# Kernel tuning notes

Measured on AMD Instinct MI355X. Metric: run time of the kernel, lower is better.

The kernel has to match this reference:

```python
import jax, jax.numpy as jnp
import numpy as np

D_MODEL = 128
H = 256          # lstm_hidden_dim
L = 2            # lstm_num_layers
PRED_LEN = 45
OUT_DIM = 2
B = 4096


def _glorot(key, shape):
    fan = shape[-1]
    return jax.random.uniform(key, shape, jnp.float32, -1.0, 1.0) / jnp.sqrt(jnp.float32(fan))


def setup_inputs() -> dict:
    key = jax.random.key(0)
    ks = jax.random.split(key, 20)
    inp = {
        "encoder_feat": jax.random.normal(ks[0], (B, D_MODEL), jnp.float32),
        "last_obs_pos": jax.random.normal(ks[1], (B, OUT_DIM), jnp.float32),
        "context": jax.random.normal(ks[2], (B, D_MODEL), jnp.float32),
        # hidden/cell init projections: Linear(d_model -> H*L)
        "Wh_init": _glorot(ks[3], (H * L, D_MODEL)),
        "bh_init": jnp.zeros((H * L,), jnp.float32),
        "Wc_init": _glorot(ks[4], (H * L, D_MODEL)),
        "bc_init": jnp.zeros((H * L,), jnp.float32),
        # LSTM layer 0: input = OUT_DIM + D_MODEL
        "W_ih0": _glorot(ks[5], (4 * H, OUT_DIM + D_MODEL)),
        "W_hh0": _glorot(ks[6], (4 * H, H)),
        "b_ih0": jnp.zeros((4 * H,), jnp.float32),
        "b_hh0": jnp.zeros((4 * H,), jnp.float32),
        # LSTM layer 1: input = H
        "W_ih1": _glorot(ks[7], (4 * H, H)),
        "W_hh1": _glorot(ks[8], (4 * H, H)),
        "b_ih1": jnp.zeros((4 * H,), jnp.float32),
        "b_hh1": jnp.zeros((4 * H,), jnp.float32),
        # output_proj: Linear(H,64) -> ReLU -> Linear(64, OUT_DIM)
        "Wp1": _glorot(ks[9], (64, H)),
        "bp1": jnp.zeros((64,), jnp.float32),
        "Wp2": _glorot(ks[10], (OUT_DIM, 64)),
        "bp2": jnp.zeros((OUT_DIM,), jnp.float32),
    }
    return inp


def _lstm_cell(gates_x, h, c, W_hh):
    # gates_x already = x @ W_ih.T + b_ih + b_hh ; torch gate order: i, f, g, o
    gates = gates_x + h @ W_hh.T
    i, f, g, o = jnp.split(gates, 4, axis=-1)
    c_new = jax.nn.sigmoid(f) * c + jax.nn.sigmoid(i) * jnp.tanh(g)
    h_new = jax.nn.sigmoid(o) * jnp.tanh(c_new)
    return h_new, c_new


def reference(encoder_feat, last_obs_pos, context,
              Wh_init, bh_init, Wc_init, bc_init,
              W_ih0, W_hh0, b_ih0, b_hh0,
              W_ih1, W_hh1, b_ih1, b_hh1,
              Wp1, bp1, Wp2, bp2):
    b = encoder_feat.shape[0]
    # init hidden/cell: [B, L*H] -> per-layer [B, H]
    h_all = (encoder_feat @ Wh_init.T + bh_init).reshape(b, L, H)
    c_all = (encoder_feat @ Wc_init.T + bc_init).reshape(b, L, H)
    h0, h1 = h_all[:, 0], h_all[:, 1]
    c0, c1 = c_all[:, 0], c_all[:, 1]

    # context is constant across steps: precompute its gate contribution once
    bias0 = b_ih0 + b_hh0
    gates_ctx = context @ W_ih0[:, OUT_DIM:].T + bias0   # [B, 4H]
    W_pos = W_ih0[:, :OUT_DIM]                            # [4H, 2]
    bias1 = b_ih1 + b_hh1

    def step(carry, _):
        pos, h0, c0, h1, c1 = carry
        gates_x0 = gates_ctx + pos @ W_pos.T
        h0, c0 = _lstm_cell(gates_x0, h0, c0, W_hh0)
        gates_x1 = h0 @ W_ih1.T + bias1
        h1, c1 = _lstm_cell(gates_x1, h1, c1, W_hh1)
        delta = jax.nn.relu(h1 @ Wp1.T + bp1) @ Wp2.T + bp2
        pos = pos + delta
        return (pos, h0, c0, h1, c1), pos

    _, traj = jax.lax.scan(step, (last_obs_pos, h0, c0, h1, c1), None, length=PRED_LEN)
    return jnp.transpose(traj, (1, 0, 2))  # [B, pred_len, 2]
```

## Files before the change

### kernel.cpp

```cpp
#include <hip/hip_runtime.h>


#define HN    256
#define DM    128
#define NSTEP 45

#define H0A_OFF  1605632ULL
#define HBUF_B   2097152ULL
#define H0B_OFF  (H0A_OFF + HBUF_B)
#define H1A_OFF  (H0B_OFF + HBUF_B)
#define H1B_OFF  (H1A_OFF + HBUF_B)
#define GX_OFF   (H1B_OFF + HBUF_B)
#define GX_B     8388608ULL
#define C0_OFF   (GX_OFF + GX_B)
#define CB_B     4194304ULL
#define C1_OFF   (C0_OFF + CB_B)
#define POSA_OFF (C1_OFF + CB_B)
#define POSB_OFF (POSA_OFF + 32768ULL)
#define WS_NEED  (POSB_OFF + 32768ULL)

typedef __attribute__((ext_vector_type(8))) short s8v;
typedef __attribute__((ext_vector_type(4))) float f32x4;

#define MFMA16(a,b,c) __builtin_amdgcn_mfma_f32_16x16x32_bf16((a),(b),(c),0,0,0)

__device__ __forceinline__ unsigned short f2bf(float f){
  union { float f; unsigned u; } x; x.f = f;
  unsigned r = x.u + 0x7fffu + ((x.u >> 16) & 1u);
  return (unsigned short)(r >> 16);
}
__device__ __forceinline__ float bf2f(unsigned short h){
  union { unsigned u; float f; } x; x.u = ((unsigned)h) << 16;
  return x.f;
}
__device__ __forceinline__ float sigm(float x){
  x = fminf(40.f, fmaxf(-40.f, x));
  return 1.f/(1.f + __expf(-x));
}
__device__ __forceinline__ float tanhx(float x){
  float xx = fminf(15.f, fmaxf(-15.f, x));
  float e = __expf(2.f*xx);
  return (e-1.f)/(e+1.f);
}

__device__ __forceinline__ void store_h(unsigned short* buf, int blk, int b, int u, float v){
  buf[(size_t)blk*4096 + (u>>5)*512 + ((b&15) + ((u>>3)&3)*16)*8 + (u&7)] = f2bf(v);
}
__device__ __forceinline__ s8v ld_af(const unsigned short* buf, int blk, int kt, int lane){
  return *(const s8v*)(buf + (size_t)blk*4096 + kt*512 + lane*8);
}

__global__ void repack(const float* __restrict__ Whh0, const float* __restrict__ Wih1,
                       const float* __restrict__ Whh1, const float* __restrict__ Wp1,
                       unsigned short* __restrict__ dst){
  int gid  = blockIdx.x*256 + threadIdx.x;
  int lane = gid & 63;
  int tile = gid >> 6;
  const float* src; int row; size_t doff;
  int k0 = (lane>>4)*8;
  if (tile < 1536){
    int mi = tile / 512;
    int r  = tile % 512;
    int ut = r & 15;
    int kt = (r >> 4) & 7;
    int g  = r >> 7;
    src  = (mi==0) ? Whh0 : (mi==1) ? Wih1 : Whh1;
    row  = g*256 + ut*16 + (lane&15);
    k0  += kt*32;
    doff = (size_t)mi*262144 + (size_t)r*512 + lane*8;
  } else {
    int r2 = tile - 1536;
    int kt = r2 & 7, pt = r2 >> 3;
    src  = Wp1;
    row  = pt*16 + (lane&15);
    k0  += kt*32;
    doff = 786432 + (size_t)r2*512 + lane*8;
  }
  const float* s = src + (size_t)row*HN + k0;
  float4 a = *(const float4*)(s);
  float4 b = *(const float4*)(s+4);
  unsigned short* d = dst + doff;
  d[0]=f2bf(a.x); d[1]=f2bf(a.y); d[2]=f2bf(a.z); d[3]=f2bf(a.w);
  d[4]=f2bf(b.x); d[5]=f2bf(b.y); d[6]=f2bf(b.z); d[7]=f2bf(b.w);
}

__global__ __launch_bounds__(512, 1)
void k_init(const float* __restrict__ enc, const float* __restrict__ pos0,
            const float* __restrict__ ctx, const float* __restrict__ Wh,
            const float* __restrict__ bh,  const float* __restrict__ Wc,
            const float* __restrict__ bc,  const float* __restrict__ Wih0,
            const float* __restrict__ bih0,const float* __restrict__ bhh0,
            unsigned short* __restrict__ h0a, unsigned short* __restrict__ h1a,
            unsigned short* __restrict__ gxg,
            float* __restrict__ c0g, float* __restrict__ c1g,
            float* __restrict__ posg)
{
  __shared__ float sh_x[16*DM];
  const int tid = threadIdx.x;
  const int blk = blockIdx.x;
  const int gb0 = blk*16;

  {
    const float4* src = (const float4*)(enc + (size_t)gb0*DM);
    ((float4*)sh_x)[tid] = src[tid];
  }
  if (tid < 32) posg[(size_t)gb0*2 + tid] = pos0[(size_t)gb0*2 + tid];
  __syncthreads();

  {
    const int r = tid;
    float ah[16], ac[16];
    #pragma unroll
    for (int b=0;b<16;b++){ ah[b]=0.f; ac[b]=0.f; }
    const float4* whr = (const float4*)(Wh + (size_t)r*DM);
    const float4* wcr = (const float4*)(Wc + (size_t)r*DM);
    #pragma unroll 4
    for (int kk=0; kk<DM/4; kk++){
      float4 w0 = whr[kk], w1 = wcr[kk];
      #pragma unroll
      for (int b=0;b<16;b++){
        float4 x = *(const float4*)&sh_x[b*DM + kk*4];
        ah[b] += w0.x*x.x + w0.y*x.y + w0.z*x.z + w0.w*x.w;
        ac[b] += w1.x*x.x + w1.y*x.y + w1.z*x.z + w1.w*x.w;
      }
    }
    float bhv = bh[r], bcv = bc[r];
    if (r < HN){
      #pragma unroll
      for (int b=0;b<16;b++){
        store_h(h0a, blk, b, r, ah[b] + bhv);
        c0g[(size_t)blk*4096 + r*16 + b] = ac[b] + bcv;
      }
    } else {
      #pragma unroll
      for (int b=0;b<16;b++){
        store_h(h1a, blk, b, r-HN, ah[b] + bhv);
        c1g[(size_t)blk*4096 + (r-HN)*16 + b] = ac[b] + bcv;
      }
    }
  }
  __syncthreads();

  {
    const float4* src = (const float4*)(ctx + (size_t)gb0*DM);
    ((float4*)sh_x)[tid] = src[tid];
  }
  __syncthreads();

  {
    float a0[16], a1[16];
    #pragma unroll
    for (int b=0;b<16;b++){ a0[b]=0.f; a1[b]=0.f; }
    const float2* wr0 = (const float2*)(Wih0 + (size_t)tid*130 + 2);
    const float2* wr1 = (const float2*)(Wih0 + (size_t)(tid+512)*130 + 2);
    #pragma unroll 4
    for (int kk=0; kk<DM/2; kk++){
      float2 w0 = wr0[kk], w1 = wr1[kk];
      #pragma unroll
      for (int b=0;b<16;b++){
        float2 x = *(const float2*)&sh_x[b*DM + kk*2];
        a0[b] += w0.x*x.x + w0.y*x.y;
        a1[b] += w1.x*x.x + w1.y*x.y;
      }
    }
    float cb0 = bih0[tid]     + bhh0[tid];
    float cb1 = bih0[tid+512] + bhh0[tid+512];
    #pragma unroll
    for (int b=0;b<16;b++){
      gxg[(size_t)blk*16384 + (size_t)tid*16 + b]       = f2bf(a0[b] + cb0);
      gxg[(size_t)blk*16384 + (size_t)(tid+512)*16 + b] = f2bf(a1[b] + cb1);
    }
  }
}

__global__ __launch_bounds__(512, 1)
void k_layer0(const unsigned short* __restrict__ wsW,
              const unsigned short* __restrict__ gxg,
              const unsigned short* __restrict__ h0rd,
              unsigned short* __restrict__ h0wr,
              const unsigned short* __restrict__ h1prev,
              float* __restrict__ c0g,
              const float* __restrict__ posRd,
              float* __restrict__ posWr,
              const float* __restrict__ Wih0,
              const float* __restrict__ bp1,
              const float* __restrict__ Wp2,
              const float* __restrict__ bp2,
              float* __restrict__ out, int t)
{
  const int tid  = threadIdx.x;
  const int lane = tid & 63;
  const int w    = tid >> 6;
  const int wb   = w >> 1;
  const int wh   = w & 1;
  const int col  = lane & 15;
  const int hi   = lane >> 4;
  const int bt   = blockIdx.x >> 3;
  const int sl   = blockIdx.x & 7;

  const int blk0 = bt*8 + wb*2;
  const int ut   = sl*2 + wh;
  const int u    = ut*16 + col;

  float p0[2][4], p1[2][4];
  if (t > 0){
    float bpv[4], w2a[4], w2b[4];
    #pragma unroll
    for (int n=0;n<4;n++){
      bpv[n] = bp1[n*16 + col];
      w2a[n] = Wp2[n*16 + col];
      w2b[n] = Wp2[64 + n*16 + col];
    }
    const float bp20 = bp2[0], bp21 = bp2[1];
    #pragma unroll
    for (int m2=0;m2<2;m2++){
      const int blk = blk0 + m2;
      f32x4 hp[4];
      #pragma unroll
      for (int n=0;n<4;n++)
        #pragma unroll
        for (int q=0;q<4;q++) hp[n][q] = bpv[n];
      #pragma unroll
      for (int kt=0;kt<8;kt++){
        s8v a = ld_af(h1prev, blk, kt, lane);
        #pragma unroll
        for (int n=0;n<4;n++){
          s8v bf = *(const s8v*)(wsW + 786432 + (size_t)(n*8+kt)*512 + lane*8);
          hp[n] = MFMA16(a, bf, hp[n]);
        }
      }
      #pragma unroll
      for (int q=0;q<4;q++){
        float s0 = 0.f, s1 = 0.f;
        #pragma unroll
        for (int n=0;n<4;n++){
          float r = fmaxf(hp[n][q], 0.f);
          s0 += r*w2a[n]; s1 += r*w2b[n];
        }
        #pragma unroll
        for (int off=1; off<16; off<<=1){
          s0 += __shfl_xor(s0, off, 64);
          s1 += __shfl_xor(s1, off, 64);
        }
        int b = blk*16 + hi*4 + q;
        float2 pp = *(const float2*)(posRd + (size_t)b*2);
        float np0 = pp.x + s0 + bp2[0];
        float np1 = pp.y + s1 + bp2[1];
        (void)bp20; (void)bp21;
        p0[m2][q] = np0; p1[m2][q] = np1;
        if (sl == 0 && wh == 0 && col == 0){
          posWr[(size_t)b*2]     = np0;
          posWr[(size_t)b*2 + 1] = np1;
          out[((size_t)b*NSTEP + (t-1))*2]     = np0;
          out[((size_t)b*NSTEP + (t-1))*2 + 1] = np1;
        }
      }
    }
  } else {
    #pragma unroll
    for (int m2=0;m2<2;m2++)
      #pragma unroll
      for (int q=0;q<4;q++){
        float2 pp = *(const float2*)(posRd + (size_t)((blk0+m2)*16 + hi*4 + q)*2);
        p0[m2][q] = pp.x; p1[m2][q] = pp.y;
      }
  }

  float wpr[4][2];
  #pragma unroll
  for (int g=0;g<4;g++){
    int row = g*256 + u;
    wpr[g][0] = Wih0[(size_t)row*130 + 0];
    wpr[g][1] = Wih0[(size_t)row*130 + 1];
  }

  f32x4 acc[2][4];
  #pragma unroll
  for (int m2=0;m2<2;m2++){
    const int blk = blk0 + m2;
    #pragma unroll
    for (int g=0;g<4;g++){
      int row = g*256 + u;
      const unsigned short* gp = gxg + (size_t)blk*16384 + (size_t)row*16 + hi*4;
      #pragma unroll
      for (int q=0;q<4;q++)
        acc[m2][g][q] = bf2f(gp[q]) + p0[m2][q]*wpr[g][0] + p1[m2][q]*wpr[g][1];
    }
  }

  #pragma unroll
  for (int kt=0;kt<8;kt++){
    s8v a0 = ld_af(h0rd, blk0,   kt, lane);
    s8v a1 = ld_af(h0rd, blk0+1, kt, lane);
    #pragma unroll
    for (int g=0;g<4;g++){
      const int r = (g*8 + kt)*16 + ut;
      s8v bf = *(const s8v*)(wsW + (size_t)r*512 + lane*8);
      acc[0][g] = MFMA16(a0, bf, acc[0][g]);
      acc[1][g] = MFMA16(a1, bf, acc[1][g]);
    }
  }

  #pragma unroll
  for (int m2=0;m2<2;m2++){
    const int blk = blk0 + m2;
    float* cp = c0g + (size_t)blk*4096 + u*16 + hi*4;
    float4 cold = *(const float4*)cp;
    float4 cnew;
    #pragma unroll
    for (int q=0;q<4;q++){
      float iv = sigm(acc[m2][0][q]);
      float fv = sigm(acc[m2][1][q]);
      float gv = tanhx(acc[m2][2][q]);
      float ov = sigm(acc[m2][3][q]);
      float cv = fv*((&cold.x)[q]) + iv*gv;
      (&cnew.x)[q] = cv;
      store_h(h0wr, blk, hi*4+q, u, ov*tanhx(cv));
    }
    *(float4*)cp = cnew;
  }
}

__global__ __launch_bounds__(512, 1)
void k_layer1(const unsigned short* __restrict__ wsW,
              const unsigned short* __restrict__ h0n,
              const unsigned short* __restrict__ h1rd,
              unsigned short* __restrict__ h1wr,
              float* __restrict__ c1g,
              const float* __restrict__ bih1,
              const float* __restrict__ bhh1)
{
  const int tid  = threadIdx.x;
  const int lane = tid & 63;
  const int w    = tid >> 6;
  const int wb   = w >> 1;
  const int wh   = w & 1;
  const int col  = lane & 15;
  const int hi   = lane >> 4;
  const int bt   = blockIdx.x >> 3;
  const int sl   = blockIdx.x & 7;

  const int blk0 = bt*8 + wb*2;
  const int ut   = sl*2 + wh;
  const int u    = ut*16 + col;

  f32x4 acc[2][4];
  #pragma unroll
  for (int g=0;g<4;g++){
    int row = g*256 + u;
    float bv = bih1[row] + bhh1[row];
    #pragma unroll
    for (int q=0;q<4;q++){ acc[0][g][q] = bv; acc[1][g][q] = bv; }
  }

  #pragma unroll
  for (int kt=0;kt<8;kt++){
    s8v a0 = ld_af(h0n, blk0,   kt, lane);
    s8v a1 = ld_af(h0n, blk0+1, kt, lane);
    #pragma unroll
    for (int g=0;g<4;g++){
      const int r = (g*8 + kt)*16 + ut;
      s8v bf = *(const s8v*)(wsW + 262144 + (size_t)r*512 + lane*8);
      acc[0][g] = MFMA16(a0, bf, acc[0][g]);
      acc[1][g] = MFMA16(a1, bf, acc[1][g]);
    }
  }
  #pragma unroll
  for (int kt=0;kt<8;kt++){
    s8v a0 = ld_af(h1rd, blk0,   kt, lane);
    s8v a1 = ld_af(h1rd, blk0+1, kt, lane);
    #pragma unroll
    for (int g=0;g<4;g++){
      const int r = (g*8 + kt)*16 + ut;
      s8v bf = *(const s8v*)(wsW + 524288 + (size_t)r*512 + lane*8);
      acc[0][g] = MFMA16(a0, bf, acc[0][g]);
      acc[1][g] = MFMA16(a1, bf, acc[1][g]);
    }
  }

  #pragma unroll
  for (int m2=0;m2<2;m2++){
    const int blk = blk0 + m2;
    float* cp = c1g + (size_t)blk*4096 + u*16 + hi*4;
    float4 cold = *(const float4*)cp;
    float4 cnew;
    #pragma unroll
    for (int q=0;q<4;q++){
      float iv = sigm(acc[m2][0][q]);
      float fv = sigm(acc[m2][1][q]);
      float gv = tanhx(acc[m2][2][q]);
      float ov = sigm(acc[m2][3][q]);
      float cv = fv*((&cold.x)[q]) + iv*gv;
      (&cnew.x)[q] = cv;
      store_h(h1wr, blk, hi*4+q, u, ov*tanhx(cv));
    }
    *(float4*)cp = cnew;
  }
}

__global__ __launch_bounds__(256, 2)
void k_head(const unsigned short* __restrict__ wsW,
            const unsigned short* __restrict__ h1n,
            const float* __restrict__ posRd,
            const float* __restrict__ bp1,
            const float* __restrict__ Wp2,
            const float* __restrict__ bp2,
            float* __restrict__ out, int t)
{
  const int tid  = threadIdx.x;
  const int lane = tid & 63;
  const int w    = tid >> 6;
  const int col  = lane & 15;
  const int hi   = lane >> 4;
  const int bt   = blockIdx.x;

  float bpv[4], w2a[4], w2b[4];
  #pragma unroll
  for (int n=0;n<4;n++){
    bpv[n] = bp1[n*16 + col];
    w2a[n] = Wp2[n*16 + col];
    w2b[n] = Wp2[64 + n*16 + col];
  }
  const float bp20 = bp2[0], bp21 = bp2[1];

  #pragma unroll
  for (int m2=0;m2<2;m2++){
    const int blk = bt*8 + w*2 + m2;
    f32x4 acc[4];
    #pragma unroll
    for (int n=0;n<4;n++)
      #pragma unroll
      for (int q=0;q<4;q++) acc[n][q] = bpv[n];
    #pragma unroll
    for (int kt=0;kt<8;kt++){
      s8v a = ld_af(h1n, blk, kt, lane);
      #pragma unroll
      for (int n=0;n<4;n++){
        s8v bf = *(const s8v*)(wsW + 786432 + (size_t)(n*8+kt)*512 + lane*8);
        acc[n] = MFMA16(a, bf, acc[n]);
      }
    }
    #pragma unroll
    for (int q=0;q<4;q++){
      float s0 = 0.f, s1 = 0.f;
      #pragma unroll
      for (int n=0;n<4;n++){
        float r = fmaxf(acc[n][q], 0.f);
        s0 += r*w2a[n]; s1 += r*w2b[n];
      }
      #pragma unroll
      for (int off=1; off<16; off<<=1){
        s0 += __shfl_xor(s0, off, 64);
        s1 += __shfl_xor(s1, off, 64);
      }
      if (col == 0){
        int b = blk*16 + hi*4 + q;
        out[((size_t)b*NSTEP + t)*2]     = posRd[(size_t)b*2]     + s0 + bp20;
        out[((size_t)b*NSTEP + t)*2 + 1] = posRd[(size_t)b*2 + 1] + s1 + bp21;
      }
    }
  }
}

extern "C" void kernel_launch(void* const* d_in, const int* in_sizes, int n_in,
                              void* d_out, int out_size, void* d_ws, size_t ws_size,
                              hipStream_t stream) {
  const float* enc  = (const float*)d_in[0];
  const float* pos0 = (const float*)d_in[1];
  const float* ctx  = (const float*)d_in[2];
  const float* Wh   = (const float*)d_in[3];
  const float* bh   = (const float*)d_in[4];
  const float* Wc   = (const float*)d_in[5];
  const float* bc   = (const float*)d_in[6];
  const float* Wih0 = (const float*)d_in[7];
  const float* Whh0 = (const float*)d_in[8];
  const float* bih0 = (const float*)d_in[9];
  const float* bhh0 = (const float*)d_in[10];
  const float* Wih1 = (const float*)d_in[11];
  const float* Whh1 = (const float*)d_in[12];
  const float* bih1 = (const float*)d_in[13];
  const float* bhh1 = (const float*)d_in[14];
  const float* Wp1  = (const float*)d_in[15];
  const float* bp1  = (const float*)d_in[16];
  const float* Wp2  = (const float*)d_in[17];
  const float* bp2  = (const float*)d_in[18];
  float* out = (float*)d_out;
  unsigned short* wsW = (unsigned short*)d_ws;

  unsigned short* h0a = (unsigned short*)((char*)d_ws + H0A_OFF);
  unsigned short* h0b = (unsigned short*)((char*)d_ws + H0B_OFF);
  unsigned short* h1a = (unsigned short*)((char*)d_ws + H1A_OFF);
  unsigned short* h1b = (unsigned short*)((char*)d_ws + H1B_OFF);
  unsigned short* gxg = (unsigned short*)((char*)d_ws + GX_OFF);
  float* c0g  = (float*)((char*)d_ws + C0_OFF);
  float* c1g  = (float*)((char*)d_ws + C1_OFF);
  float* posA = (float*)((char*)d_ws + POSA_OFF);
  float* posB = (float*)((char*)d_ws + POSB_OFF);

  hipLaunchKernelGGL(repack, dim3(392), dim3(256), 0, stream,
                     Whh0, Wih1, Whh1, Wp1, wsW);

  hipLaunchKernelGGL(k_init, dim3(256), dim3(512), 0, stream,
                     enc, pos0, ctx, Wh, bh, Wc, bc, Wih0, bih0, bhh0,
                     h0a, h1a, gxg, c0g, c1g, posA);

  unsigned short* h1prev = h1a;
  for (int t = 0; t < NSTEP; t++){
    unsigned short* h0r = (t & 1) ? h0b : h0a;
    unsigned short* h0w = (t & 1) ? h0a : h0b;
    unsigned short* h1r = (t & 1) ? h1b : h1a;
    unsigned short* h1w = (t & 1) ? h1a : h1b;
    float* posRead  = (t == 0) ? posA : ((t & 1) ? posA : posB);
    float* posWrite = (t & 1) ? posB : posA;

    hipLaunchKernelGGL(k_layer0, dim3(256), dim3(512), 0, stream,
                       wsW, gxg, h0r, h0w, h1prev, c0g,
                       posRead, posWrite, Wih0, bp1, Wp2, bp2, out, t);
    hipLaunchKernelGGL(k_layer1, dim3(256), dim3(512), 0, stream,
                       wsW, h0w, h1r, h1w, c1g, bih1, bhh1);
    h1prev = h1w;
  }
  hipLaunchKernelGGL(k_head, dim3(32), dim3(256), 0, stream,
                     wsW, h1prev, posA, bp1, Wp2, bp2, out, NSTEP-1);
}
```

Baseline: 1.840 ms.

## Interleave recurrent and projection MFMAs and remap block indices for weight locality

Block index mapping is swapped so that consecutive blocks share the same hidden-unit slice (sl) rather than the same batch tile, which changes which weight tiles neighbouring workgroups read at the same time, in the hope of better cache sharing. In layer 0 the output-projection MFMAs for the previous step's h1 are interleaved with the h0 recurrent MFMAs in a single k-loop. The gx/pos input contribution is moved after the MMA into the activation stage. In layer 1 the two k-loops (input and recurrent) are fused into one loop. This gives more independent MFMA chains per iteration to hide latency, at the cost of higher register pressure from the extra live accumulators.

```diff
diff --git a/kernel.cpp b/kernel.cpp
--- a/kernel.cpp
+++ b/kernel.cpp
@@ -195,14 +195,23 @@
   const int wh   = w & 1;
   const int col  = lane & 15;
   const int hi   = lane >> 4;
-  const int bt   = blockIdx.x >> 3;
-  const int sl   = blockIdx.x & 7;
+  const int bt   = blockIdx.x & 31;
+  const int sl   = blockIdx.x >> 5;
 
   const int blk0 = bt*8 + wb*2;
   const int ut   = sl*2 + wh;
   const int u    = ut*16 + col;
 
+  f32x4 acc[2][4];
+  #pragma unroll
+  for (int m2=0;m2<2;m2++)
+    #pragma unroll
+    for (int g=0;g<4;g++)
+      #pragma unroll
+      for (int q=0;q<4;q++) acc[m2][g][q] = 0.f;
+
   float p0[2][4], p1[2][4];
+
   if (t > 0){
     float bpv[4], w2a[4], w2b[4];
     #pragma unroll
@@ -211,30 +220,42 @@
       w2a[n] = Wp2[n*16 + col];
       w2b[n] = Wp2[64 + n*16 + col];
     }
+    f32x4 hp[2][4];
+    #pragma unroll
+    for (int m2=0;m2<2;m2++)
+      #pragma unroll
+      for (int n=0;n<4;n++)
+        #pragma unroll
+        for (int q=0;q<4;q++) hp[m2][n][q] = bpv[n];
+
+    #pragma unroll
+    for (int kt=0;kt<8;kt++){
+      s8v a0 = ld_af(h0rd,   blk0,   kt, lane);
+      s8v a1 = ld_af(h0rd,   blk0+1, kt, lane);
+      s8v b0 = ld_af(h1prev, blk0,   kt, lane);
+      s8v b1 = ld_af(h1prev, blk0+1, kt, lane);
+      #pragma unroll
+      for (int g=0;g<4;g++){
+        const int r = (g*8 + kt)*16 + ut;
+        s8v bf = *(const s8v*)(wsW + (size_t)r*512 + lane*8);
+        acc[0][g] = MFMA16(a0, bf, acc[0][g]);
+        acc[1][g] = MFMA16(a1, bf, acc[1][g]);
+        s8v wf = *(const s8v*)(wsW + 786432 + (size_t)(g*8+kt)*512 + lane*8);
+        hp[0][g] = MFMA16(b0, wf, hp[0][g]);
+        hp[1][g] = MFMA16(b1, wf, hp[1][g]);
+      }
+    }
+
     const float bp20 = bp2[0], bp21 = bp2[1];
     #pragma unroll
     for (int m2=0;m2<2;m2++){
       const int blk = blk0 + m2;
-      f32x4 hp[4];
-      #pragma unroll
-      for (int n=0;n<4;n++)
-        #pragma unroll
-        for (int q=0;q<4;q++) hp[n][q] = bpv[n];
-      #pragma unroll
-      for (int kt=0;kt<8;kt++){
-        s8v a = ld_af(h1prev, blk, kt, lane);
-        #pragma unroll
-        for (int n=0;n<4;n++){
-          s8v bf = *(const s8v*)(wsW + 786432 + (size_t)(n*8+kt)*512 + lane*8);
-          hp[n] = MFMA16(a, bf, hp[n]);
-        }
-      }
       #pragma unroll
       for (int q=0;q<4;q++){
         float s0 = 0.f, s1 = 0.f;
         #pragma unroll
         for (int n=0;n<4;n++){
-          float r = fmaxf(hp[n][q], 0.f);
+          float r = fmaxf(hp[m2][n][q], 0.f);
           s0 += r*w2a[n]; s1 += r*w2b[n];
         }
         #pragma unroll
@@ -244,9 +265,8 @@
         }
         int b = blk*16 + hi*4 + q;
         float2 pp = *(const float2*)(posRd + (size_t)b*2);
-        float np0 = pp.x + s0 + bp2[0];
-        float np1 = pp.y + s1 + bp2[1];
-        (void)bp20; (void)bp21;
+        float np0 = pp.x + s0 + bp20;
+        float np1 = pp.y + s1 + bp21;
         p0[m2][q] = np0; p1[m2][q] = np1;
         if (sl == 0 && wh == 0 && col == 0){
           posWr[(size_t)b*2]     = np0;
@@ -258,6 +278,18 @@
     }
   } else {
     #pragma unroll
+    for (int kt=0;kt<8;kt++){
+      s8v a0 = ld_af(h0rd, blk0,   kt, lane);
+      s8v a1 = ld_af(h0rd, blk0+1, kt, lane);
+      #pragma unroll
+      for (int g=0;g<4;g++){
+        const int r = (g*8 + kt)*16 + ut;
+        s8v bf = *(const s8v*)(wsW + (size_t)r*512 + lane*8);
+        acc[0][g] = MFMA16(a0, bf, acc[0][g]);
+        acc[1][g] = MFMA16(a1, bf, acc[1][g]);
+      }
+    }
+    #pragma unroll
     for (int m2=0;m2<2;m2++)
       #pragma unroll
       for (int q=0;q<4;q++){
@@ -273,34 +305,6 @@
     wpr[g][0] = Wih0[(size_t)row*130 + 0];
     wpr[g][1] = Wih0[(size_t)row*130 + 1];
   }
-
-  f32x4 acc[2][4];
-  #pragma unroll
-  for (int m2=0;m2<2;m2++){
-    const int blk = blk0 + m2;
-    #pragma unroll
-    for (int g=0;g<4;g++){
-      int row = g*256 + u;
-      const unsigned short* gp = gxg + (size_t)blk*16384 + (size_t)row*16 + hi*4;
-      #pragma unroll
-      for (int q=0;q<4;q++)
-        acc[m2][g][q] = bf2f(gp[q]) + p0[m2][q]*wpr[g][0] + p1[m2][q]*wpr[g][1];
-    }
-  }
-
-  #pragma unroll
-  for (int kt=0;kt<8;kt++){
-    s8v a0 = ld_af(h0rd, blk0,   kt, lane);
-    s8v a1 = ld_af(h0rd, blk0+1, kt, lane);
-    #pragma unroll
-    for (int g=0;g<4;g++){
-      const int r = (g*8 + kt)*16 + ut;
-      s8v bf = *(const s8v*)(wsW + (size_t)r*512 + lane*8);
-      acc[0][g] = MFMA16(a0, bf, acc[0][g]);
-      acc[1][g] = MFMA16(a1, bf, acc[1][g]);
-    }
-  }
-
   #pragma unroll
   for (int m2=0;m2<2;m2++){
     const int blk = blk0 + m2;
@@ -309,10 +313,16 @@
     float4 cnew;
     #pragma unroll
     for (int q=0;q<4;q++){
-      float iv = sigm(acc[m2][0][q]);
-      float fv = sigm(acc[m2][1][q]);
-      float gv = tanhx(acc[m2][2][q]);
-      float ov = sigm(acc[m2][3][q]);
+      float gate[4];
+      #pragma unroll
+      for (int g=0;g<4;g++){
+        const unsigned short* gp = gxg + (size_t)blk*16384 + (size_t)(g*256+u)*16 + hi*4;
+        gate[g] = acc[m2][g][q] + bf2f(gp[q]) + p0[m2][q]*wpr[g][0] + p1[m2][q]*wpr[g][1];
+      }
+      float iv = sigm(gate[0]);
+      float fv = sigm(gate[1]);
+      float gv = tanhx(gate[2]);
+      float ov = sigm(gate[3]);
       float cv = fv*((&cold.x)[q]) + iv*gv;
       (&cnew.x)[q] = cv;
       store_h(h0wr, blk, hi*4+q, u, ov*tanhx(cv));
@@ -337,8 +347,8 @@
   const int wh   = w & 1;
   const int col  = lane & 15;
   const int hi   = lane >> 4;
-  const int bt   = blockIdx.x >> 3;
-  const int sl   = blockIdx.x & 7;
+  const int bt   = blockIdx.x & 31;
+  const int sl   = blockIdx.x >> 5;
 
   const int blk0 = bt*8 + wb*2;
   const int ut   = sl*2 + wh;
@@ -355,26 +365,19 @@
 
   #pragma unroll
   for (int kt=0;kt<8;kt++){
-    s8v a0 = ld_af(h0n, blk0,   kt, lane);
-    s8v a1 = ld_af(h0n, blk0+1, kt, lane);
+    s8v x0 = ld_af(h0n,  blk0,   kt, lane);
+    s8v x1 = ld_af(h0n,  blk0+1, kt, lane);
+    s8v y0 = ld_af(h1rd, blk0,   kt, lane);
+    s8v y1 = ld_af(h1rd, blk0+1, kt, lane);
     #pragma unroll
     for (int g=0;g<4;g++){
       const int r = (g*8 + kt)*16 + ut;
-      s8v bf = *(const s8v*)(wsW + 262144 + (size_t)r*512 + lane*8);
-      acc[0][g] = MFMA16(a0, bf, acc[0][g]);
-      acc[1][g] = MFMA16(a1, bf, acc[1][g]);
-    }
-  }
-  #pragma unroll
-  for (int kt=0;kt<8;kt++){
-    s8v a0 = ld_af(h1rd, blk0,   kt, lane);
-    s8v a1 = ld_af(h1rd, blk0+1, kt, lane);
-    #pragma unroll
-    for (int g=0;g<4;g++){
-      const int r = (g*8 + kt)*16 + ut;
-      s8v bf = *(const s8v*)(wsW + 524288 + (size_t)r*512 + lane*8);
-      acc[0][g] = MFMA16(a0, bf, acc[0][g]);
-      acc[1][g] = MFMA16(a1, bf, acc[1][g]);
+      s8v b1v = *(const s8v*)(wsW + 262144 + (size_t)r*512 + lane*8);
+      acc[0][g] = MFMA16(x0, b1v, acc[0][g]);
+      acc[1][g] = MFMA16(x1, b1v, acc[1][g]);
+      s8v b2v = *(const s8v*)(wsW + 524288 + (size_t)r*512 + lane*8);
+      acc[0][g] = MFMA16(y0, b2v, acc[0][g]);
+      acc[1][g] = MFMA16(y1, b2v, acc[1][g]);
     }
   }
 
```

Measured after the change: 1.867 ms. Within noise of the previous version (+1.5%).
